# Performance work log

Measured on AMD Instinct MI355X. Metric: run time of the kernel, lower is better.

The kernel has to match this reference:

```python
import jax, jax.numpy as jnp
import numpy as np
import math

B, H, S, D = 2, 16, 2048, 72
D12 = D // 12  # freq dim per head per component
L_PREFIX, L_SEQ = 576, 512
THETA_T = 100.0


def _make_freqs():
    n = H * D12
    log_min, log_max = math.log(math.pi), math.log(10.0 * math.pi)
    f = jnp.exp(jnp.linspace(log_min, log_max, n + 1)[:-1])  # (H*D12,)
    freqs = jnp.stack([f, f]).reshape(2, D12, H)
    freqs = jnp.swapaxes(freqs, -1, -2)  # (2, H, D12)
    t = THETA_T ** (-jnp.arange(n, dtype=jnp.float32) / n)
    t_freqs = t.reshape(D12, H).T  # (H, D12)
    return freqs.astype(jnp.float32), t_freqs.astype(jnp.float32)


def setup_inputs() -> dict:
    key = jax.random.key(0)
    ks = jax.random.split(key, 8)
    freqs, t_freqs = _make_freqs()
    return {
        "q": jax.random.normal(ks[0], (B, H, S, D), dtype=jnp.float32),
        "k": jax.random.normal(ks[1], (B, H, S, D), dtype=jnp.float32),
        "v": jax.random.normal(ks[2], (B, H, S, D), dtype=jnp.float32),
        "pos": jax.random.uniform(ks[3], (B, S, 2), dtype=jnp.float32),
        "pos_orig": jax.random.uniform(ks[4], (B, S, 2), dtype=jnp.float32),
        "time": jax.random.uniform(ks[5], (B, S), dtype=jnp.float32),
        "freqs": freqs,
        "t_freqs": t_freqs,
        "scale": jax.random.uniform(ks[6], (H, 1, 1), dtype=jnpp_f32()) if False else jax.random.uniform(ks[6], (H, 1, 1), dtype=jnp.float32) + 0.5,
        "l_prefix": L_PREFIX,
        "l_seq": L_SEQ,
    }


def jnp_f32():
    return jnp.float32


def _fp_rope_theta(pos, pos_orig, time, freqs, t_freqs):
    # FPRoPE.forward: theta per token, per head. (B,S,H,5*D12)
    p = jnp.stack([pos_orig, pos], axis=2) * 2.0 - 1.0  # (B,S,2,2)
    th_w = p[..., 0][:, :, :, None, None] * freqs[0]  # (B,S,2,H,D12)
    th_h = p[..., 1][:, :, :, None, None] * freqs[1]  # (B,S,2,H,D12)
    th_t = time[:, :, None, None, None] * t_freqs      # (B,S,1,H,D12)
    theta = jnp.concatenate([th_h, th_w, th_t], axis=2)  # (B,S,5,H,D12)
    theta = jnp.transpose(theta, (0, 3, 1, 2, 4)).reshape(B, H, S, 5 * D12)
    return theta


def _apply_rotary(x, theta):
    d = theta.shape[-1]
    x1, x2, x3 = x[..., :d], x[..., d:2 * d], x[..., 2 * d:]
    c, s = jnp.cos(theta), jnp.sin(theta)
    return jnp.concatenate([x1 * c - x2 * s, x2 * c + x1 * s, x3], axis=-1)


def _block_mask(l_prefix, l_seq):
    # inference_query_causal_mask_mod: prefix attends to nothing; pokes causal;
    # queries attend to prefix+pokes (and self via qn==kn).
    idx = jnp.arange(S)
    qn = (idx - l_prefix)[:, None]
    kn = (idx - l_prefix)[None, :]
    return (qn >= 0) & ((qn == kn) | ((qn >= kn) & (qn < l_seq)) | ((kn < l_seq) & (qn >= l_seq)))


def reference(q, k, v, pos, pos_orig, time, freqs, t_freqs, scale, l_prefix, l_seq):
    theta = _fp_rope_theta(pos, pos_orig, time, freqs, t_freqs)
    q = _apply_rotary(q, theta)
    k = _apply_rotary(k, theta)
    # cosine-similarity QK rescaling (scale_for_cosine_sim)
    eps = 1e-6
    ss = jnp.sqrt(scale)  # (H,1,1) broadcasts over (B,H,S,1)
    q = q * (ss * jax.lax.rsqrt(jnp.sum(q * q, axis=-1, keepdims=True) + eps))
    k = k * (ss * jax.lax.rsqrt(jnp.sum(k * k, axis=-1, keepdims=True) + eps))
    mask = _block_mask(l_prefix, l_seq)  # (S,S)
    scores = jnp.einsum('bhqd,bhkd->bhqk', q, k)
    scores = jnp.where(mask, scores, jnp.float32(-1e30))
    probs = jax.nn.softmax(scores, axis=-1)
    # fully-masked rows (prefix queries) output zeros, matching flex_attention
    row_valid = jnp.any(mask, axis=-1)  # (S,)
    probs = jnp.where(row_valid[None, None, :, None], probs, 0.0)
    return jnp.einsum('bhqk,bhkd->bhqd', probs, v)
```

## Files before the change

kernel.cpp:

```cpp
#include <hip/hip_runtime.h>
#include <math.h>

#define B_ 2
#define H_ 16
#define S_ 2048
#define D_ 72
#define LP 576
#define WEND 1088
#define DP 96
#define DV 80
#define NQ (S_ - LP)

#define NPREP2 (B_ * H_ * S_ / 8)
#define NVT    (32 * B_ * H_)

typedef __bf16 bf16x8 __attribute__((ext_vector_type(8)));
typedef float f32x4 __attribute__((ext_vector_type(4)));
typedef short sh4   __attribute__((ext_vector_type(4)));

static __device__ __forceinline__ unsigned pack2bf(float a, float b) {
    __bf16 x = (__bf16)a, y = (__bf16)b;
    unsigned short ux = __builtin_bit_cast(unsigned short, x);
    unsigned short uy = __builtin_bit_cast(unsigned short, y);
    return (unsigned)ux | ((unsigned)uy << 16);
}

static __device__ __forceinline__ f32x4 mfma32(bf16x8 a, bf16x8 b, f32x4 c) {
    return __builtin_amdgcn_mfma_f32_16x16x32_bf16(a, b, c, 0, 0, 0);
}
static __device__ __forceinline__ f32x4 mfma16k(sh4 a, sh4 b, f32x4 c) {
    return __builtin_amdgcn_mfma_f32_16x16x16bf16_1k(a, b, c, 0, 0, 0);
}
static __device__ __forceinline__ void gll16(const void* g, void* l) {
    __builtin_amdgcn_global_load_lds((const __attribute__((address_space(1))) unsigned*)g,
                                     (__attribute__((address_space(3))) unsigned*)l, 16, 0, 0);
}

__global__ __launch_bounds__(256) void pre_kernel(
    const float* __restrict__ q, const float* __restrict__ k,
    const float* __restrict__ v,
    const float* __restrict__ pos, const float* __restrict__ pos_orig,
    const float* __restrict__ time_, const float* __restrict__ freqs,
    const float* __restrict__ t_freqs, const float* __restrict__ scale,
    unsigned* __restrict__ qn, unsigned* __restrict__ kn,
    unsigned short* __restrict__ vt, float* __restrict__ out)
{
    __shared__ __align__(16) float tile[64 * 77];
    if (blockIdx.x < NPREP2) {
        unsigned short* shp = (unsigned short*)tile;
        const int wave = threadIdx.x >> 6;
        const int lane = threadIdx.x & 63;
        const int j = lane & 31;
        const int rw = wave * 2 + (lane >> 5);
        const int row = blockIdx.x * 8 + rw;
        const int s = row & (S_ - 1);
        const int h = (row >> 11) & (H_ - 1);
        const int b = row >> 15;
        const long base = (long)row * D_;
        const int p2 = (b * S_ + s) * 2;

        float oq1 = 0.f, oq2 = 0.f, ok1 = 0.f, ok2 = 0.f;
        float pq[6], pk[6];
        float ssq = 0.f, ssk = 0.f;
        if (j < 30) {
            const float x1q = q[base + j], x2q = q[base + j + 30];
            const float x1k = k[base + j], x2k = k[base + j + 30];
            const int g = j / 6, i = j - 6 * g;
            const float fh = freqs[96 + h * 6 + i];
            const float fw = freqs[h * 6 + i];
            const float ft = t_freqs[h * 6 + i];
            const float f  = (g < 2) ? fh : ((g < 4) ? fw : ft);
            const float by_o = pos_orig[p2 + 1] * 2.f - 1.f;
            const float by_p = pos[p2 + 1]      * 2.f - 1.f;
            const float bx_o = pos_orig[p2 + 0] * 2.f - 1.f;
            const float bx_p = pos[p2 + 0]      * 2.f - 1.f;
            const float bt   = time_[b * S_ + s];
            const float bv = (g == 0) ? by_o : (g == 1) ? by_p :
                             (g == 2) ? bx_o : (g == 3) ? bx_p : bt;
            float sn, cs;
            __sincosf(bv * f, &sn, &cs);
            oq1 = x1q * cs - x2q * sn;  oq2 = x2q * cs + x1q * sn;
            ok1 = x1k * cs - x2k * sn;  ok2 = x2k * cs + x1k * sn;
            ssq = oq1 * oq1 + oq2 * oq2;
            ssk = ok1 * ok1 + ok2 * ok2;
        } else {
            const int e0 = 60 + 6 * (j - 30);
            #pragma unroll
            for (int m = 0; m < 3; ++m) {
                const float2 a = *(const float2*)(q + base + e0 + 2 * m);
                const float2 c = *(const float2*)(k + base + e0 + 2 * m);
                pq[2 * m] = a.x; pq[2 * m + 1] = a.y;
                pk[2 * m] = c.x; pk[2 * m + 1] = c.y;
                ssq += a.x * a.x + a.y * a.y;
                ssk += c.x * c.x + c.y * c.y;
            }
        }
        #pragma unroll
        for (int m = 1; m < 32; m <<= 1) { ssq += __shfl_xor(ssq, m); ssk += __shfl_xor(ssk, m); }
        const float ss = sqrtf(scale[h]);
        const float fq = ss * rsqrtf(ssq + 1e-6f);
        const float fk = ss * rsqrtf(ssk + 1e-6f);

        unsigned short* sq_ = shp + rw * 96;
        unsigned short* sk_ = shp + 768 + rw * 96;
        if (j < 30) {
            sq_[j]      = __builtin_bit_cast(unsigned short, (__bf16)(oq1 * fq));
            sq_[j + 30] = __builtin_bit_cast(unsigned short, (__bf16)(oq2 * fq));
            sk_[j]      = __builtin_bit_cast(unsigned short, (__bf16)(ok1 * fk));
            sk_[j + 30] = __builtin_bit_cast(unsigned short, (__bf16)(ok2 * fk));
        } else {
            const int e0 = 60 + 6 * (j - 30);
            #pragma unroll
            for (int m = 0; m < 6; ++m) {
                sq_[e0 + m] = __builtin_bit_cast(unsigned short, (__bf16)(pq[m] * fq));
                sk_[e0 + m] = __builtin_bit_cast(unsigned short, (__bf16)(pk[m] * fk));
            }
        }
        __syncthreads();
        const int t = threadIdx.x;
        if (t < 192) {
            const int arr = t / 96, rem = t - arr * 96;
            const int rr = rem / 12, seg = rem - rr * 12;
            uint4 val = make_uint4(0u, 0u, 0u, 0u);
            if (seg < 9) val = ((const uint4*)(shp + arr * 768 + rr * 96))[seg];
            unsigned* dst = (arr ? kn : qn) + ((long)(blockIdx.x * 8 + rr)) * 48;
            ((uint4*)dst)[seg] = val;
        }
    } else {
        const int bx2 = blockIdx.x - NPREP2;
        const int st = bx2 & 31, bh = bx2 >> 5;
        const int s0 = st * 64;
        const int t = threadIdx.x;
        if (st < 9) {
            float4* o4 = (float4*)(out + (long)(bh * S_ + s0) * D_);
            for (int i = t; i < 1152; i += 256) o4[i] = make_float4(0.f, 0.f, 0.f, 0.f);
        }
        for (int i = t; i < 1152; i += 256) {
            const int r = i / 18, c = i - r * 18;
            const float4 g = ((const float4*)v)[((long)(bh * S_ + s0 + r) * 18) + c];
            float* d = &tile[r * 77 + c * 4];
            d[0] = g.x; d[1] = g.y; d[2] = g.z; d[3] = g.w;
        }
        __syncthreads();
        for (int i = t; i < 1280; i += 256) {
            const int dd = i >> 4, s4 = i & 15;
            float f0 = 0.f, f1 = 0.f, f2 = 0.f, f3 = 0.f;
            if (dd < D_) {
                f0 = tile[(s4 * 4 + 0) * 77 + dd];
                f1 = tile[(s4 * 4 + 1) * 77 + dd];
                f2 = tile[(s4 * 4 + 2) * 77 + dd];
                f3 = tile[(s4 * 4 + 3) * 77 + dd];
            }
            uint2 o; o.x = pack2bf(f0, f1); o.y = pack2bf(f2, f3);
            ((uint2*)vt)[((((long)bh * DV + dd) << 11) + s0 + s4 * 4) >> 2] = o;
        }
    }
}

__global__ __launch_bounds__(64) void attn_kernel(
    const unsigned short* __restrict__ qn, const unsigned short* __restrict__ kn,
    const unsigned short* __restrict__ vt, float* __restrict__ out)
{
    __shared__ __align__(16) unsigned stage[2][2816];

    const int bh = blockIdx.y;
    const int qw0 = LP + blockIdx.x * 32;
    const int lane = threadIdx.x & 63;
    const int quad = lane >> 4, l16 = lane & 15;
    const bool causal = (qw0 < WEND);
    const int nt = causal ? (qw0 / 32 + 1) : (WEND / 32);

    const unsigned short* qn_b = qn + (((long)bh) << 11) * DP;
    const unsigned short* kn_b = kn + (((long)bh) << 11) * DP;
    const unsigned short* vt_b = vt + (long)bh * DV * S_;

    bf16x8 qf[2][3];
    #pragma unroll
    for (int m = 0; m < 2; ++m)
        #pragma unroll
        for (int c = 0; c < 3; ++c)
            qf[m][c] = *(const bf16x8*)(qn_b + (long)(qw0 + 16 * m + l16) * DP + c * 32 + quad * 8);

    f32x4 o[2][5];
    float den[2] = {0.f, 0.f};
    #pragma unroll
    for (int m = 0; m < 2; ++m)
        #pragma unroll
        for (int dt = 0; dt < 5; ++dt) { o[m][dt][0]=0.f; o[m][dt][1]=0.f; o[m][dt][2]=0.f; o[m][dt][3]=0.f; }

    const unsigned short* pk[6];
    const unsigned short* pv[5];
    #pragma unroll
    for (int g = 0; g < 2; ++g)
        #pragma unroll
        for (int c = 0; c < 3; ++c)
            pk[g * 3 + c] = kn_b + (long)(16 * g + l16) * DP + c * 32 + quad * 8;
    #pragma unroll
    for (int dt = 0; dt < 5; ++dt)
        pv[dt] = vt_b + (((long)(dt * 16 + l16)) << 11) + quad * 8;

#define STAGE(BUF) do {                                                     \
    _Pragma("unroll")                                                       \
    for (int i_ = 0; i_ < 6; ++i_) {                                        \
        gll16(pk[i_], (void*)&(BUF)[i_ * 256]);                             \
        pk[i_] += 32 * DP;                                                  \
    }                                                                       \
    _Pragma("unroll")                                                       \
    for (int i_ = 0; i_ < 5; ++i_) {                                        \
        gll16(pv[i_], (void*)&(BUF)[(6 + i_) * 256]);                       \
        pv[i_] += 32;                                                       \
    }                                                                       \
} while (0)

    const int voffV = ((quad >> 1) * 16 + l16) * 8 + (quad & 1) * 4;
    const int qa0 = qw0 + l16;

    STAGE(stage[0]);

    for (int t = 0; t < nt; ++t) {
        const unsigned short* sb = (const unsigned short*)stage[t & 1];
        asm volatile("s_waitcnt lgkmcnt(0)" ::: "memory");
        if (t + 1 < nt) {
            STAGE(stage[(t + 1) & 1]);
            asm volatile("s_waitcnt vmcnt(11)" ::: "memory");
        } else {
            asm volatile("s_waitcnt vmcnt(0)" ::: "memory");
        }

        bf16x8 kf[2][3];
        #pragma unroll
        for (int g = 0; g < 2; ++g)
            #pragma unroll
            for (int c = 0; c < 3; ++c)
                kf[g][c] = *(const bf16x8*)(sb + (g * 3 + c) * 512 + lane * 8);
        sh4 vf[2][5];
        #pragma unroll
        for (int g = 0; g < 2; ++g)
            #pragma unroll
            for (int dt = 0; dt < 5; ++dt)
                vf[g][dt] = *(const sh4*)(sb + 3072 + dt * 512 + g * 256 + voffV);

        const bool maskedLast = causal && (t == nt - 1);
        const int kb = t * 32;

        #pragma unroll
        for (int m = 0; m < 2; ++m) {
            f32x4 s0, s1;
            s0[0]=0.f; s0[1]=0.f; s0[2]=0.f; s0[3]=0.f;
            s1[0]=0.f; s1[1]=0.f; s1[2]=0.f; s1[3]=0.f;
            __builtin_amdgcn_s_setprio(1);
            #pragma unroll
            for (int c = 0; c < 3; ++c) {
                s0 = mfma32(kf[0][c], qf[m][c], s0);
                s1 = mfma32(kf[1][c], qf[m][c], s1);
            }
            __builtin_amdgcn_s_setprio(0);
            const int qa = qa0 + 16 * m;
            #pragma unroll
            for (int g = 0; g < 2; ++g) {
                const f32x4 sg = g ? s1 : s0;
                sh4 pa;
                #pragma unroll
                for (int r = 0; r < 4; ++r) {
                    float e = __expf(sg[r]);
                    if (maskedLast) {
                        const int ka = kb + 16 * g + quad * 4 + r;
                        if (ka > qa) e = 0.f;
                    }
                    const __bf16 pb = (__bf16)e;
                    den[m] += (float)pb;
                    pa[r] = __builtin_bit_cast(short, pb);
                }
                __builtin_amdgcn_s_setprio(1);
                #pragma unroll
                for (int dt = 0; dt < 5; ++dt)
                    o[m][dt] = mfma16k(pa, vf[g][dt], o[m][dt]);
                __builtin_amdgcn_s_setprio(0);
            }
        }
    }
#undef STAGE

    float pd[2] = {0.f, 0.f};
    if (!causal) {
        #pragma unroll
        for (int m = 0; m < 2; ++m) {
            float sp = 0.f;
            #pragma unroll
            for (int c = 0; c < 3; ++c) {
                const bf16x8 kd = *(const bf16x8*)(kn_b + (long)(qw0 + 16 * m + l16) * DP + c * 32 + quad * 8);
                #pragma unroll
                for (int j = 0; j < 8; ++j) sp += (float)qf[m][c][j] * (float)kd[j];
            }
            sp += __shfl_xor(sp, 16);
            sp += __shfl_xor(sp, 32);
            pd[m] = __expf(sp);
        }
    }

    float denf[2];
    #pragma unroll
    for (int m = 0; m < 2; ++m) {
        float d = den[m];
        d += __shfl_xor(d, 16);
        d += __shfl_xor(d, 32);
        denf[m] = causal ? d : (d + pd[m]);
    }

    #pragma unroll
    for (int m = 0; m < 2; ++m) {
        #pragma unroll
        for (int r = 0; r < 4; ++r) {
            const int row = 16 * m + quad * 4 + r;
            const float df = __shfl(denf[m], quad * 4 + r);
            const float inv = 1.f / df;
            const int qa = qw0 + row;
            float* orow = out + ((long)(bh * S_ + qa)) * D_;
            float pdr = 0.f;
            if (!causal) pdr = __shfl(pd[m], quad * 4 + r);
            #pragma unroll
            for (int dt = 0; dt < 5; ++dt) {
                float val = o[m][dt][r];
                if (!causal) {
                    const unsigned short uv = vt_b[(((long)(dt * 16 + l16)) << 11) + qa];
                    val += pdr * (float)__builtin_bit_cast(__bf16, uv);
                }
                const int dim = dt * 16 + l16;
                if (dim < D_) orow[dim] = val * inv;
            }
        }
    }
}

extern "C" void kernel_launch(void* const* d_in, const int* in_sizes, int n_in,
                              void* d_out, int out_size, void* d_ws, size_t ws_size,
                              hipStream_t stream) {
    const float* q        = (const float*)d_in[0];
    const float* k        = (const float*)d_in[1];
    const float* v        = (const float*)d_in[2];
    const float* pos      = (const float*)d_in[3];
    const float* pos_orig = (const float*)d_in[4];
    const float* time_    = (const float*)d_in[5];
    const float* freqs    = (const float*)d_in[6];
    const float* t_freqs  = (const float*)d_in[7];
    const float* scale    = (const float*)d_in[8];
    float* out = (float*)d_out;

    unsigned* qn = (unsigned*)d_ws;
    unsigned* kn = qn + (size_t)B_ * H_ * S_ * 48;
    unsigned short* vt = (unsigned short*)(kn + (size_t)B_ * H_ * S_ * 48);

    pre_kernel<<<dim3(NPREP2 + NVT), dim3(256), 0, stream>>>(
        q, k, v, pos, pos_orig, time_, freqs, t_freqs, scale, qn, kn, vt, out);
    attn_kernel<<<dim3(NQ / 32, B_ * H_), dim3(64), 0, stream>>>(
        (const unsigned short*)qn, (const unsigned short*)kn, vt, out);
}
```

Measured before the change: 187.9 us.

## Share K/V tile staging across two waves per block with XCD-aware scheduling

Attention blocks grow from one wave covering 32 queries to two waves covering 64 queries. The two waves alternate issuing async K/V tile loads into a 4-deep shared ring, separated by barriers, so each K/V tile is fetched once per 64 queries instead of once per 32. Block IDs are remapped so that consecutive blocks spread across the 8 XCDs. The log2(e) factor is folded into the q normalisation so the kernel can use exp2f. The cost is a per-tile barrier and the causal mask now evaluated on every tile.

```diff
diff --git a/kernel.cpp b/kernel.cpp
--- a/kernel.cpp
+++ b/kernel.cpp
@@ -13,6 +13,10 @@
 
 #define NPREP2 (B_ * H_ * S_ / 8)
 #define NVT    (32 * B_ * H_)
+
+#define NQB64 (NQ / 64)
+#define NWG2 (NQB64 * B_ * H_)
+#define WPX2 (NWG2 / 8)
 
 typedef __bf16 bf16x8 __attribute__((ext_vector_type(8)));
 typedef float f32x4 __attribute__((ext_vector_type(4)));
@@ -98,7 +102,7 @@
         #pragma unroll
         for (int m = 1; m < 32; m <<= 1) { ssq += __shfl_xor(ssq, m); ssk += __shfl_xor(ssk, m); }
         const float ss = sqrtf(scale[h]);
-        const float fq = ss * rsqrtf(ssq + 1e-6f);
+        const float fq = ss * rsqrtf(ssq + 1e-6f) * 1.44269504088896340736f;
         const float fk = ss * rsqrtf(ssk + 1e-6f);
 
         unsigned short* sq_ = shp + rw * 96;
@@ -157,18 +161,23 @@
     }
 }
 
-__global__ __launch_bounds__(64) void attn_kernel(
+__global__ __launch_bounds__(128) void attn_kernel(
     const unsigned short* __restrict__ qn, const unsigned short* __restrict__ kn,
     const unsigned short* __restrict__ vt, float* __restrict__ out)
 {
-    __shared__ __align__(16) unsigned stage[2][2816];
-
-    const int bh = blockIdx.y;
-    const int qw0 = LP + blockIdx.x * 32;
+    __shared__ __align__(16) unsigned stage4[4][2816];
+
+    const int id = blockIdx.x;
+    const int vlin = (id & 7) * WPX2 + (id >> 3);
+    const int bh = vlin / NQB64;
+    const int bx = vlin - bh * NQB64;
+    const int qw0 = LP + bx * 64;
+    const int w = threadIdx.x >> 6;
     const int lane = threadIdx.x & 63;
     const int quad = lane >> 4, l16 = lane & 15;
+    const int qw = qw0 + 32 * w;
     const bool causal = (qw0 < WEND);
-    const int nt = causal ? (qw0 / 32 + 1) : (WEND / 32);
+    const int nt = causal ? (qw0 / 32 + 2) : (WEND / 32);
 
     const unsigned short* qn_b = qn + (((long)bh) << 11) * DP;
     const unsigned short* kn_b = kn + (((long)bh) << 11) * DP;
@@ -179,7 +188,7 @@
     for (int m = 0; m < 2; ++m)
         #pragma unroll
         for (int c = 0; c < 3; ++c)
-            qf[m][c] = *(const bf16x8*)(qn_b + (long)(qw0 + 16 * m + l16) * DP + c * 32 + quad * 8);
+            qf[m][c] = *(const bf16x8*)(qn_b + (long)(qw + 16 * m + l16) * DP + c * 32 + quad * 8);
 
     f32x4 o[2][5];
     float den[2] = {0.f, 0.f};
@@ -194,38 +203,41 @@
     for (int g = 0; g < 2; ++g)
         #pragma unroll
         for (int c = 0; c < 3; ++c)
-            pk[g * 3 + c] = kn_b + (long)(16 * g + l16) * DP + c * 32 + quad * 8;
+            pk[g * 3 + c] = kn_b + (long)(32 * w + 16 * g + l16) * DP + c * 32 + quad * 8;
     #pragma unroll
     for (int dt = 0; dt < 5; ++dt)
-        pv[dt] = vt_b + (((long)(dt * 16 + l16)) << 11) + quad * 8;
+        pv[dt] = vt_b + (((long)(dt * 16 + l16)) << 11) + 32 * w + quad * 8;
 
 #define STAGE(BUF) do {                                                     \
     _Pragma("unroll")                                                       \
     for (int i_ = 0; i_ < 6; ++i_) {                                        \
         gll16(pk[i_], (void*)&(BUF)[i_ * 256]);                             \
-        pk[i_] += 32 * DP;                                                  \
+        pk[i_] += 64 * DP;                                                  \
     }                                                                       \
     _Pragma("unroll")                                                       \
     for (int i_ = 0; i_ < 5; ++i_) {                                        \
         gll16(pv[i_], (void*)&(BUF)[(6 + i_) * 256]);                       \
-        pv[i_] += 32;                                                       \
+        pv[i_] += 64;                                                       \
     }                                                                       \
 } while (0)
 
     const int voffV = ((quad >> 1) * 16 + l16) * 8 + (quad & 1) * 4;
-    const int qa0 = qw0 + l16;
-
-    STAGE(stage[0]);
+    const int qa0 = qw + l16;
+
+    STAGE(stage4[w]);
 
     for (int t = 0; t < nt; ++t) {
-        const unsigned short* sb = (const unsigned short*)stage[t & 1];
+        const unsigned short* sb = (const unsigned short*)stage4[t & 3];
         asm volatile("s_waitcnt lgkmcnt(0)" ::: "memory");
-        if (t + 1 < nt) {
-            STAGE(stage[(t + 1) & 1]);
-            asm volatile("s_waitcnt vmcnt(11)" ::: "memory");
-        } else {
-            asm volatile("s_waitcnt vmcnt(0)" ::: "memory");
-        }
+        if ((t & 1) == w) {
+            if (t + 2 < nt) {
+                STAGE(stage4[(t + 2) & 3]);
+                asm volatile("s_waitcnt vmcnt(11)" ::: "memory");
+            } else {
+                asm volatile("s_waitcnt vmcnt(0)" ::: "memory");
+            }
+        }
+        __builtin_amdgcn_s_barrier();
 
         bf16x8 kf[2][3];
         #pragma unroll
@@ -240,7 +252,6 @@
             for (int dt = 0; dt < 5; ++dt)
                 vf[g][dt] = *(const sh4*)(sb + 3072 + dt * 512 + g * 256 + voffV);
 
-        const bool maskedLast = causal && (t == nt - 1);
         const int kb = t * 32;
 
         #pragma unroll
@@ -262,8 +273,8 @@
                 sh4 pa;
                 #pragma unroll
                 for (int r = 0; r < 4; ++r) {
-                    float e = __expf(sg[r]);
-                    if (maskedLast) {
+                    float e = exp2f(sg[r]);
+                    if (causal) {
                         const int ka = kb + 16 * g + quad * 4 + r;
                         if (ka > qa) e = 0.f;
                     }
@@ -288,13 +299,13 @@
             float sp = 0.f;
             #pragma unroll
             for (int c = 0; c < 3; ++c) {
-                const bf16x8 kd = *(const bf16x8*)(kn_b + (long)(qw0 + 16 * m + l16) * DP + c * 32 + quad * 8);
+                const bf16x8 kd = *(const bf16x8*)(kn_b + (long)(qw + 16 * m + l16) * DP + c * 32 + quad * 8);
                 #pragma unroll
                 for (int j = 0; j < 8; ++j) sp += (float)qf[m][c][j] * (float)kd[j];
             }
             sp += __shfl_xor(sp, 16);
             sp += __shfl_xor(sp, 32);
-            pd[m] = __expf(sp);
+            pd[m] = exp2f(sp);
         }
     }
 
@@ -314,7 +325,7 @@
             const int row = 16 * m + quad * 4 + r;
             const float df = __shfl(denf[m], quad * 4 + r);
             const float inv = 1.f / df;
-            const int qa = qw0 + row;
+            const int qa = qw + row;
             float* orow = out + ((long)(bh * S_ + qa)) * D_;
             float pdr = 0.f;
             if (!causal) pdr = __shfl(pd[m], quad * 4 + r);
@@ -352,6 +363,6 @@
 
     pre_kernel<<<dim3(NPREP2 + NVT), dim3(256), 0, stream>>>(
         q, k, v, pos, pos_orig, time_, freqs, t_freqs, scale, qn, kn, vt, out);
-    attn_kernel<<<dim3(NQ / 32, B_ * H_), dim3(64), 0, stream>>>(
+    attn_kernel<<<dim3(NWG2), dim3(128), 0, stream>>>(
         (const unsigned short*)qn, (const unsigned short*)kn, vt, out);
 }
```

New measurement: 185.4 us. About the same (-1.4%).
